# Kernel tuning notes

Measured on AMD Instinct MI355X. Metric: run time of the kernel, lower is better.

Reference implementation:

```python
import jax, jax.numpy as jnp
import numpy as np
import math

V, S, D, B = 50257, 2048, 512, 4
DFF = 4 * D
EPS = 1e-5


def layer_norm(z, g, b):
    mu = jnp.mean(z, axis=-1, keepdims=True)
    var = jnp.mean((z - mu) ** 2, axis=-1, keepdims=True)
    return (z - mu) * jax.lax.rsqrt(var + EPS) * g + b


def pos_embedding(seq_len, d_model):
    # Faithful to get_positional_value: angle = pos / 10000**(2*i/d), sin for even i, cos for odd i
    pos = jnp.arange(seq_len, dtype=jnp.float32)[:, None]          # [S,1]
    i = jnp.arange(d_model, dtype=jnp.float32)[None, :]            # [1,D]
    ang = pos / jnp.power(10000.0, 2.0 * i / d_model)              # [S,D]
    even = (jnp.arange(d_model) % 2 == 0)[None, :]
    return jnp.where(even, jnp.sin(ang), jnp.cos(ang))


def setup_inputs() -> dict:
    key = jax.random.key(0)
    ks = jax.random.split(key, 14)
    w = lambda k, sh: jax.random.normal(k, sh, dtype=jnp.float32) * 0.02
    return {
        "input_seq": jax.random.randint(ks[0], (B, S), 0, V),
        "emb": w(ks[1], (V, D)),
        "wk": w(ks[2], (D, D)), "bk": jnp.zeros((D,), jnp.float32),
        "wq": w(ks[3], (D, D)), "bq": jnp.zeros((D,), jnp.float32),
        "wv": w(ks[4], (D, D)), "bv": jnp.zeros((D,), jnp.float32),
        "ln_g": jnp.ones((D,), jnp.float32), "ln_b": jnp.zeros((D,), jnp.float32),
        "w1": w(ks[5], (D, DFF)), "b1": jnp.zeros((DFF,), jnp.float32),
        "w2": w(ks[6], (DFF, D)), "b2": jnp.zeros((D,), jnp.float32),
    }


def reference(input_seq, emb, wk, bk, wq, bq, wv, bv, ln_g, ln_b, w1, b1, w2, b2):
    x = emb[input_seq]                                              # [B,S,D]
    x = (x + pos_embedding(S, D)) * math.sqrt(D)
    # NB original passes (k, q, v) into Attention(Q, K, V), so Q:=k_proj, K:=q_proj, V:=v_proj
    k = x @ wk + bk
    q = x @ wq + bq
    v = x @ wv + bv
    scores = jnp.einsum("bid,bjd->bij", k, q) / math.sqrt(D)        # [B,S,S]
    attn = jax.nn.softmax(scores, axis=-1) @ v                      # [B,S,D]
    r = layer_norm(x + attn, ln_g, ln_b)
    ff = jax.nn.gelu(r @ w1 + b1, approximate=False) @ w2 + b2
    out = layer_norm(r + ff, ln_g, ln_b)                            # shared LN params (same module reused)
    return out
```

## Files before the change

### kernel.cpp

```cpp
#include <hip/hip_runtime.h>
#include <math.h>

static constexpr int BB  = 4;
static constexpr int S   = 2048;
static constexpr int D   = 512;
static constexpr int DFF = 2048;
static constexpr int BS  = BB * S;

using v8h = __attribute__((ext_vector_type(8))) _Float16;
using v4h = __attribute__((ext_vector_type(4))) _Float16;
using v2h = __attribute__((ext_vector_type(2))) _Float16;
using v4f = __attribute__((ext_vector_type(4))) float;

__device__ __forceinline__ void async16(const void* g, void* l) {
  __builtin_amdgcn_global_load_lds(
      (const __attribute__((address_space(1))) unsigned int*)g,
      (__attribute__((address_space(3))) unsigned int*)l, 16, 0, 0);
}

__device__ __forceinline__ float blockSum(float v) {
#pragma unroll
  for (int o = 32; o; o >>= 1) v += __shfl_xor(v, o, 64);
  __shared__ float t[4];
  __syncthreads();
  if ((threadIdx.x & 63) == 0) t[threadIdx.x >> 6] = v;
  __syncthreads();
  return t[0] + t[1] + t[2] + t[3];
}
__device__ __forceinline__ float blockMax(float v) {
#pragma unroll
  for (int o = 32; o; o >>= 1) v = fmaxf(v, __shfl_xor(v, o, 64));
  __shared__ float t[4];
  __syncthreads();
  if ((threadIdx.x & 63) == 0) t[threadIdx.x >> 6] = v;
  __syncthreads();
  return fmaxf(fmaxf(t[0], t[1]), fmaxf(t[2], t[3]));
}

__global__ __launch_bounds__(256) void embed_pos_k(
    const int* __restrict__ seq, const float* __restrict__ emb,
    float* __restrict__ X, _Float16* __restrict__ Xh) {
  const int bs = blockIdx.x;
  const int s  = bs & (S - 1);
  const int idx = seq[bs];
  const float* er = emb + (size_t)idx * D;
  const float cexp = -0.05190512648261504f;
  const int d0 = threadIdx.x * 2;
  const float2 e2 = *(const float2*)&er[d0];
  const float a0 = (float)s * exp2f((float)d0 * cexp);
  const float a1 = (float)s * exp2f((float)(d0 + 1) * cexp);
  const float v0 = (e2.x + sinf(a0)) * 22.62741699796952f;
  const float v1 = (e2.y + cosf(a1)) * 22.62741699796952f;
  const size_t o = (size_t)bs * D + d0;
  *(float2*)&X[o] = make_float2(v0, v1);
  *(v2h*)&Xh[o] = v2h{(_Float16)v0, (_Float16)v1};
}

__global__ __launch_bounds__(256) void prep_k(
    const float* __restrict__ wk, const float* __restrict__ wq,
    const float* __restrict__ wv, const float* __restrict__ w1,
    const float* __restrict__ w2, const float* __restrict__ bk,
    const float* __restrict__ bq, const float* __restrict__ bv,
    _Float16* __restrict__ wcat, _Float16* __restrict__ w1T,
    _Float16* __restrict__ w2T, float* __restrict__ bcat) {
  const int idx = blockIdx.x * 256 + threadIdx.x;
  if (idx < 786432) {
    const int which = idx >> 18, e = idx & 262143;
    const int k = e >> 9, n = e & 511;
    const float* w = (which == 0) ? wk : (which == 1) ? wq : wv;
    wcat[((long)(which * 512 + n)) * 512 + k] = (_Float16)w[e];
  } else if (idx < 786432 + 1048576) {
    const int e = idx - 786432;
    const int k = e >> 11, n = e & 2047;
    w1T[(long)n * 512 + k] = (_Float16)w1[e];
  } else if (idx < 786432 + 2097152) {
    const int e = idx - 786432 - 1048576;
    const int k = e >> 9, n = e & 511;
    w2T[(long)n * 2048 + k] = (_Float16)w2[e];
  } else if (idx < 786432 + 2097152 + 1536) {
    const int e = idx - 786432 - 2097152;
    const float* b = (e < 512) ? bk : (e < 1024) ? bq : bv;
    bcat[e] = b[e & 511];
  }
}

template <int OMODE, int ACT>
__global__ __launch_bounds__(512, 2) void mm256_k(
    const _Float16* __restrict__ Ap, const _Float16* __restrict__ Bp,
    void* __restrict__ Cp, void* __restrict__ Cp2, void* __restrict__ Cp3,
    const float* __restrict__ bias,
    int N, int K, long sA, long sB, long sC, float scale) {
  constexpr int ATE = 256 * 64;
  constexpr int TILE = 2 * ATE;
  __shared__ __align__(16) _Float16 lds[2 * TILE];

  const int tid = threadIdx.x, lane = tid & 63, w = tid >> 6;
  const int quad = lane >> 4, l16 = lane & 15;
  const int wm = w >> 2, wn = w & 3;
  const int m0 = blockIdx.y * 256, n0 = blockIdx.x * 256;

  const _Float16* A = Ap + (long)blockIdx.z * sA;
  const _Float16* B = Bp + (long)blockIdx.z * sB;

  v4f acc[8][4] = {};
  const int srow8 = lane >> 3;
  const int cs = (lane & 7) ^ srow8;
  const int lsw = l16 & 7;

  auto stage = [&](int k0, int half) {
    _Float16* Ah = lds + half * TILE;
    _Float16* Bh = Ah + ATE;
#pragma unroll
    for (int i = 0; i < 4; ++i) {
      const int is = w + i * 8;
      async16(A + (long)(m0 + is * 8 + srow8) * K + k0 + cs * 8, Ah + is * 512);
      async16(B + (long)(n0 + is * 8 + srow8) * K + k0 + cs * 8, Bh + is * 512);
    }
  };

  stage(0, 0);
  __syncthreads();

  const int nK = K >> 6;
  for (int t = 0; t < nK; ++t) {
    const int cur = t & 1;
    if (t + 1 < nK) stage((t + 1) << 6, cur ^ 1);

    const _Float16* Ah = lds + cur * TILE;
    const _Float16* Bh = Ah + ATE;

    v8h bfr[4][2];
#pragma unroll
    for (int nt = 0; nt < 4; ++nt) {
      const int rn = wn * 64 + nt * 16 + l16;
#pragma unroll
      for (int kk = 0; kk < 2; ++kk) {
        const int c = (kk * 4 + quad) ^ lsw;
        bfr[nt][kk] = *(v8h*)&Bh[rn * 64 + c * 8];
      }
    }
#pragma unroll
    for (int mt = 0; mt < 8; ++mt) {
      const int rr = wm * 128 + mt * 16 + l16;
      v8h af[2];
#pragma unroll
      for (int kk = 0; kk < 2; ++kk) {
        const int c = (kk * 4 + quad) ^ lsw;
        af[kk] = *(v8h*)&Ah[rr * 64 + c * 8];
      }
#pragma unroll
      for (int kk = 0; kk < 2; ++kk)
#pragma unroll
        for (int nt = 0; nt < 4; ++nt)
          acc[mt][nt] = __builtin_amdgcn_mfma_f32_16x16x32_f16(
              af[kk], bfr[nt][kk], acc[mt][nt], 0, 0, 0);
    }

    __syncthreads();
  }

  const long Cz = (long)blockIdx.z * sC;
  const int region = n0 >> 9;
#pragma unroll
  for (int nt = 0; nt < 4; ++nt) {
    const int gn = n0 + wn * 64 + nt * 16 + l16;
    const int gnl = gn & 511;
    const float bv = bias ? bias[gn] : 0.0f;
#pragma unroll
    for (int mt = 0; mt < 8; ++mt) {
      const int gmb = m0 + wm * 128 + mt * 16 + quad * 4;
      if constexpr (OMODE == 4) {
        if (region == 2) {
          const int z2 = gmb >> 11, ml = gmb & 2047;
          v4h h4;
#pragma unroll
          for (int r = 0; r < 4; ++r)
            h4[r] = (_Float16)(acc[mt][nt][r] * scale + bv);
          *(v4h*)&((_Float16*)Cp3)[((long)z2 * 512 + gnl) * 2048 + ml] = h4;
          continue;
        }
      }
#pragma unroll
      for (int r = 0; r < 4; ++r) {
        const int gm = gmb + r;
        float v = acc[mt][nt][r] * scale + bv;
        if constexpr (ACT == 1)
          v = 0.5f * v * (1.0f + erff(v * 0.7071067811865476f));
        if constexpr (OMODE == 1) {
          ((_Float16*)Cp)[Cz + (long)gm * N + gn] = (_Float16)v;
        } else {
          if (region == 0) {
            ((_Float16*)Cp)[(long)gm * 512 + gnl] = (_Float16)v;
          } else {
            ((_Float16*)Cp2)[(long)gm * 512 + gnl] = (_Float16)v;
          }
        }
      }
    }
  }
}

template <int TM, int OMODE, int ACT>
__global__ __launch_bounds__(256) void mm_k(
    const _Float16* __restrict__ Ap, const _Float16* __restrict__ Bp,
    void* __restrict__ Cp, void* __restrict__ Cp2, void* __restrict__ Cp3,
    const float* __restrict__ bias,
    int N, int K, long sA, long sB, long sC, float scale) {
  constexpr int ATE = TM * 64;
  constexpr int BTE = 128 * 64;
  constexpr int TILE = ATE + BTE;
  __shared__ __align__(16) _Float16 lds[2 * TILE];

  const int tid = threadIdx.x, lane = tid & 63, w = tid >> 6;
  const int quad = lane >> 4, l16 = lane & 15;
  constexpr int MT = 4;
  constexpr int NT = (TM == 128) ? 4 : 2;
  constexpr int WN = (TM == 128) ? 64 : 32;
  const int wm = (TM == 128) ? (w >> 1) : 0;
  const int wn = (TM == 128) ? (w & 1) : w;
  const int m0 = blockIdx.y * TM, n0 = blockIdx.x * 128;

  const _Float16* A = Ap + (long)blockIdx.z * sA;
  const _Float16* B = Bp + (long)blockIdx.z * sB;

  v4f acc[MT][NT] = {};
  const int srow8 = lane >> 3;
  const int cs = (lane & 7) ^ srow8;
  const int lsw = l16 & 7;

  auto stage = [&](int k0, int half) {
    _Float16* Ah = lds + half * TILE;
    _Float16* Bh = Ah + ATE;
#pragma unroll
    for (int i = 0; i < TM / 32; ++i) {
      const int is = w + i * 4;
      async16(A + (long)(m0 + is * 8 + srow8) * K + k0 + cs * 8, Ah + is * 512);
    }
#pragma unroll
    for (int i = 0; i < 4; ++i) {
      const int is = w + i * 4;
      async16(B + (long)(n0 + is * 8 + srow8) * K + k0 + cs * 8, Bh + is * 512);
    }
  };

  stage(0, 0);
  __syncthreads();

  const int nK = K >> 6;
  for (int t = 0; t < nK; ++t) {
    const int cur = t & 1;
    if (t + 1 < nK) stage((t + 1) << 6, cur ^ 1);

    const _Float16* Ah = lds + cur * TILE;
    const _Float16* Bh = Ah + ATE;

    v8h af[MT][2], bfr[NT][2];
#pragma unroll
    for (int mt = 0; mt < MT; ++mt) {
      const int rr = wm * 64 + mt * 16 + l16;
#pragma unroll
      for (int kk = 0; kk < 2; ++kk) {
        const int c = (kk * 4 + quad) ^ lsw;
        af[mt][kk] = *(v8h*)&Ah[rr * 64 + c * 8];
      }
    }
#pragma unroll
    for (int nt = 0; nt < NT; ++nt) {
      const int rn = wn * WN + nt * 16 + l16;
#pragma unroll
      for (int kk = 0; kk < 2; ++kk) {
        const int c = (kk * 4 + quad) ^ lsw;
        bfr[nt][kk] = *(v8h*)&Bh[rn * 64 + c * 8];
      }
    }
#pragma unroll
    for (int kk = 0; kk < 2; ++kk)
#pragma unroll
      for (int mt = 0; mt < MT; ++mt)
#pragma unroll
        for (int nt = 0; nt < NT; ++nt)
          acc[mt][nt] = __builtin_amdgcn_mfma_f32_16x16x32_f16(
              af[mt][kk], bfr[nt][kk], acc[mt][nt], 0, 0, 0);

    __syncthreads();
  }

  const long Cz = (long)blockIdx.z * sC;
#pragma unroll
  for (int nt = 0; nt < NT; ++nt) {
    const int gn = n0 + wn * WN + nt * 16 + l16;
    const float bv = bias ? bias[gn] : 0.0f;
#pragma unroll
    for (int mt = 0; mt < MT; ++mt) {
      const int gmb = m0 + wm * 64 + mt * 16 + quad * 4;
#pragma unroll
      for (int r = 0; r < 4; ++r) {
        const int gm = gmb + r;
        float v = acc[mt][nt][r] * scale + bv;
        if constexpr (ACT == 1)
          v = 0.5f * v * (1.0f + erff(v * 0.7071067811865476f));
        if constexpr (OMODE == 0) {
          ((float*)Cp)[Cz + (long)gm * N + gn] = v;
        } else {
          ((_Float16*)Cp)[Cz + (long)gm * N + gn] = (_Float16)v;
        }
      }
    }
  }
}

__global__ __launch_bounds__(256) void softmax_k(_Float16* __restrict__ Sc) {
  _Float16* p = Sc + (size_t)blockIdx.x * S;
  const int base = threadIdx.x * 8;
  const v8h a = *(const v8h*)(p + base);
  float v[8];
#pragma unroll
  for (int i = 0; i < 8; ++i) v[i] = (float)a[i];
  float m = -1e30f;
#pragma unroll
  for (int i = 0; i < 8; ++i) m = fmaxf(m, v[i]);
  m = blockMax(m);
  float sum = 0.f;
#pragma unroll
  for (int i = 0; i < 8; ++i) {
    v[i] = exp2f((v[i] - m) * 1.44269504f);
    sum += v[i];
  }
  sum = blockSum(sum);
  const float inv = 1.0f / sum;
  v8h o;
#pragma unroll
  for (int i = 0; i < 8; ++i) o[i] = (_Float16)(v[i] * inv);
  *(v8h*)(p + base) = o;
}

__global__ __launch_bounds__(256) void ln_res_k(
    float* __restrict__ X, const float* __restrict__ Add,
    const float* __restrict__ g, const float* __restrict__ b,
    _Float16* __restrict__ rF) {
  float* xr = X + (size_t)blockIdx.x * D;
  const float* ar = Add + (size_t)blockIdx.x * D;
  _Float16* rf = rF + (size_t)blockIdx.x * D;
  const int d0 = threadIdx.x * 2;
  const float2 xv = *(const float2*)&xr[d0];
  const float2 av = *(const float2*)&ar[d0];
  const float z0 = xv.x + av.x;
  const float z1 = xv.y + av.y;
  const float mu = blockSum(z0 + z1) * (1.0f / D);
  const float dd0 = z0 - mu, dd1 = z1 - mu;
  const float var = blockSum(dd0 * dd0 + dd1 * dd1) * (1.0f / D);
  const float rs = rsqrtf(var + 1e-5f);
  const float2 gv = *(const float2*)&g[d0];
  const float2 bv = *(const float2*)&b[d0];
  const float v0 = dd0 * rs * gv.x + bv.x;
  const float v1 = dd1 * rs * gv.y + bv.y;
  *(float2*)&xr[d0] = make_float2(v0, v1);
  *(v2h*)&rf[d0] = v2h{(_Float16)v0, (_Float16)v1};
}

__global__ __launch_bounds__(256) void ln_out_k(
    const float* __restrict__ R, const float* __restrict__ F,
    const float* __restrict__ g, const float* __restrict__ b,
    float* __restrict__ out) {
  const float* rr = R + (size_t)blockIdx.x * D;
  const float* fr = F + (size_t)blockIdx.x * D;
  float* orow = out + (size_t)blockIdx.x * D;
  const int d0 = threadIdx.x * 2;
  const float2 rv = *(const float2*)&rr[d0];
  const float2 fv = *(const float2*)&fr[d0];
  const float z0 = rv.x + fv.x;
  const float z1 = rv.y + fv.y;
  const float mu = blockSum(z0 + z1) * (1.0f / D);
  const float dd0 = z0 - mu, dd1 = z1 - mu;
  const float var = blockSum(dd0 * dd0 + dd1 * dd1) * (1.0f / D);
  const float rs = rsqrtf(var + 1e-5f);
  const float2 gv = *(const float2*)&g[d0];
  const float2 bv = *(const float2*)&b[d0];
  *(float2*)&orow[d0] =
      make_float2(dd0 * rs * gv.x + bv.x, dd1 * rs * gv.y + bv.y);
}

extern "C" void kernel_launch(void* const* d_in, const int* in_sizes, int n_in,
                              void* d_out, int out_size, void* d_ws, size_t ws_size,
                              hipStream_t stream) {
  (void)in_sizes; (void)n_in; (void)out_size; (void)ws_size;
  const int*   seq = (const int*)d_in[0];
  const float* emb = (const float*)d_in[1];
  const float* wk  = (const float*)d_in[2];
  const float* bk  = (const float*)d_in[3];
  const float* wq  = (const float*)d_in[4];
  const float* bq  = (const float*)d_in[5];
  const float* wv  = (const float*)d_in[6];
  const float* bv  = (const float*)d_in[7];
  const float* lng = (const float*)d_in[8];
  const float* lnb = (const float*)d_in[9];
  const float* w1  = (const float*)d_in[10];
  const float* b1  = (const float*)d_in[11];
  const float* w2  = (const float*)d_in[12];
  const float* b2  = (const float*)d_in[13];

  const size_t MBy = 1024 * 1024;
  char* wsb = (char*)d_ws;
  float*    X    = (float*)wsb;
  _Float16* Xh   = (_Float16*)(wsb + 16 * MBy);
  _Float16* kF   = (_Float16*)(wsb + 24 * MBy);
  _Float16* qF   = (_Float16*)(wsb + 32 * MBy);
  _Float16* vT   = (_Float16*)(wsb + 40 * MBy);
  _Float16* Sc   = (_Float16*)(wsb + 48 * MBy);
  float*    attn = (float*)(wsb + 81 * MBy);
  _Float16* rF   = (_Float16*)(wsb + 24 * MBy);
  _Float16* hF   = (_Float16*)(wsb + 48 * MBy);
  float*    ff   = (float*)(wsb + 32 * MBy);
  _Float16* wcat = (_Float16*)(wsb + 100 * MBy);
  float*    bcat = (float*)(wsb + 102 * MBy);
  _Float16* w1T  = (_Float16*)(wsb + 103 * MBy);
  _Float16* w2T  = (_Float16*)(wsb + 105 * MBy);

  const long SD = (long)S * D, SSl = (long)S * S;

  prep_k<<<11270, 256, 0, stream>>>(wk, wq, wv, w1, w2, bk, bq, bv,
                                    wcat, w1T, w2T, bcat);
  embed_pos_k<<<BS, 256, 0, stream>>>(seq, emb, X, Xh);

  mm256_k<4, 0><<<dim3(6, 32, 1), 512, 0, stream>>>(
      Xh, wcat, kF, qF, vT, bcat, 1536, D, 0, 0, 0, 1.0f);

  mm256_k<1, 0><<<dim3(8, 8, BB), 512, 0, stream>>>(
      kF, qF, Sc, nullptr, nullptr, nullptr, S, D, SD, SD, SSl,
      0.044194173824159216f);

  softmax_k<<<BS, 256, 0, stream>>>(Sc);

  mm_k<64, 0, 0><<<dim3(4, 32, BB), 256, 0, stream>>>(
      Sc, vT, attn, nullptr, nullptr, nullptr, D, S, SSl, (long)D * S, SD,
      1.0f);

  ln_res_k<<<BS, 256, 0, stream>>>(X, attn, lng, lnb, rF);

  mm256_k<1, 1><<<dim3(8, 32, 1), 512, 0, stream>>>(
      rF, w1T, hF, nullptr, nullptr, b1, DFF, D, 0, 0, 0, 1.0f);
  mm_k<64, 0, 0><<<dim3(4, 128, 1), 256, 0, stream>>>(
      hF, w2T, ff, nullptr, nullptr, b2, D, DFF, 0, 0, 0, 1.0f);

  ln_out_k<<<BS, 256, 0, stream>>>(X, ff, lng, lnb, (float*)d_out);
}
```

Before: 391.2 us.

## Replace 256-tile GEMMs with 128-tile kernel and add triple-buffered K-pipelined GEMM

Removes the 512-thread 256x256-tile GEMM and routes the QKV, QK^T and FFN1 products through the 128-row mm_k kernel, which gains the fused split-output epilogue. This launches more, smaller blocks. It also adds mm64p_k, a 64x128-tile GEMM with a three-stage LDS ring and explicit vmcnt waits, used for the long-K products (attn@V and FFN2) to overlap global loads with MFMA. The trade-off is less data reuse per block in exchange for better occupancy and latency hiding.

Result: faster. 365.6 us (-6.5%).

```diff
diff --git a/kernel.cpp b/kernel.cpp
--- a/kernel.cpp
+++ b/kernel.cpp
@@ -84,122 +84,6 @@
   }
 }
 
-template <int OMODE, int ACT>
-__global__ __launch_bounds__(512, 2) void mm256_k(
-    const _Float16* __restrict__ Ap, const _Float16* __restrict__ Bp,
-    void* __restrict__ Cp, void* __restrict__ Cp2, void* __restrict__ Cp3,
-    const float* __restrict__ bias,
-    int N, int K, long sA, long sB, long sC, float scale) {
-  constexpr int ATE = 256 * 64;
-  constexpr int TILE = 2 * ATE;
-  __shared__ __align__(16) _Float16 lds[2 * TILE];
-
-  const int tid = threadIdx.x, lane = tid & 63, w = tid >> 6;
-  const int quad = lane >> 4, l16 = lane & 15;
-  const int wm = w >> 2, wn = w & 3;
-  const int m0 = blockIdx.y * 256, n0 = blockIdx.x * 256;
-
-  const _Float16* A = Ap + (long)blockIdx.z * sA;
-  const _Float16* B = Bp + (long)blockIdx.z * sB;
-
-  v4f acc[8][4] = {};
-  const int srow8 = lane >> 3;
-  const int cs = (lane & 7) ^ srow8;
-  const int lsw = l16 & 7;
-
-  auto stage = [&](int k0, int half) {
-    _Float16* Ah = lds + half * TILE;
-    _Float16* Bh = Ah + ATE;
-#pragma unroll
-    for (int i = 0; i < 4; ++i) {
-      const int is = w + i * 8;
-      async16(A + (long)(m0 + is * 8 + srow8) * K + k0 + cs * 8, Ah + is * 512);
-      async16(B + (long)(n0 + is * 8 + srow8) * K + k0 + cs * 8, Bh + is * 512);
-    }
-  };
-
-  stage(0, 0);
-  __syncthreads();
-
-  const int nK = K >> 6;
-  for (int t = 0; t < nK; ++t) {
-    const int cur = t & 1;
-    if (t + 1 < nK) stage((t + 1) << 6, cur ^ 1);
-
-    const _Float16* Ah = lds + cur * TILE;
-    const _Float16* Bh = Ah + ATE;
-
-    v8h bfr[4][2];
-#pragma unroll
-    for (int nt = 0; nt < 4; ++nt) {
-      const int rn = wn * 64 + nt * 16 + l16;
-#pragma unroll
-      for (int kk = 0; kk < 2; ++kk) {
-        const int c = (kk * 4 + quad) ^ lsw;
-        bfr[nt][kk] = *(v8h*)&Bh[rn * 64 + c * 8];
-      }
-    }
-#pragma unroll
-    for (int mt = 0; mt < 8; ++mt) {
-      const int rr = wm * 128 + mt * 16 + l16;
-      v8h af[2];
-#pragma unroll
-      for (int kk = 0; kk < 2; ++kk) {
-        const int c = (kk * 4 + quad) ^ lsw;
-        af[kk] = *(v8h*)&Ah[rr * 64 + c * 8];
-      }
-#pragma unroll
-      for (int kk = 0; kk < 2; ++kk)
-#pragma unroll
-        for (int nt = 0; nt < 4; ++nt)
-          acc[mt][nt] = __builtin_amdgcn_mfma_f32_16x16x32_f16(
-              af[kk], bfr[nt][kk], acc[mt][nt], 0, 0, 0);
-    }
-
-    __syncthreads();
-  }
-
-  const long Cz = (long)blockIdx.z * sC;
-  const int region = n0 >> 9;
-#pragma unroll
-  for (int nt = 0; nt < 4; ++nt) {
-    const int gn = n0 + wn * 64 + nt * 16 + l16;
-    const int gnl = gn & 511;
-    const float bv = bias ? bias[gn] : 0.0f;
-#pragma unroll
-    for (int mt = 0; mt < 8; ++mt) {
-      const int gmb = m0 + wm * 128 + mt * 16 + quad * 4;
-      if constexpr (OMODE == 4) {
-        if (region == 2) {
-          const int z2 = gmb >> 11, ml = gmb & 2047;
-          v4h h4;
-#pragma unroll
-          for (int r = 0; r < 4; ++r)
-            h4[r] = (_Float16)(acc[mt][nt][r] * scale + bv);
-          *(v4h*)&((_Float16*)Cp3)[((long)z2 * 512 + gnl) * 2048 + ml] = h4;
-          continue;
-        }
-      }
-#pragma unroll
-      for (int r = 0; r < 4; ++r) {
-        const int gm = gmb + r;
-        float v = acc[mt][nt][r] * scale + bv;
-        if constexpr (ACT == 1)
-          v = 0.5f * v * (1.0f + erff(v * 0.7071067811865476f));
-        if constexpr (OMODE == 1) {
-          ((_Float16*)Cp)[Cz + (long)gm * N + gn] = (_Float16)v;
-        } else {
-          if (region == 0) {
-            ((_Float16*)Cp)[(long)gm * 512 + gnl] = (_Float16)v;
-          } else {
-            ((_Float16*)Cp2)[(long)gm * 512 + gnl] = (_Float16)v;
-          }
-        }
-      }
-    }
-  }
-}
-
 template <int TM, int OMODE, int ACT>
 __global__ __launch_bounds__(256) void mm_k(
     const _Float16* __restrict__ Ap, const _Float16* __restrict__ Bp,
@@ -286,13 +170,26 @@
   }
 
   const long Cz = (long)blockIdx.z * sC;
+  const int region = n0 >> 9;
 #pragma unroll
   for (int nt = 0; nt < NT; ++nt) {
     const int gn = n0 + wn * WN + nt * 16 + l16;
+    const int gnl = gn & 511;
     const float bv = bias ? bias[gn] : 0.0f;
 #pragma unroll
     for (int mt = 0; mt < MT; ++mt) {
       const int gmb = m0 + wm * 64 + mt * 16 + quad * 4;
+      if constexpr (OMODE == 4) {
+        if (region == 2) {
+          const int z2 = gmb >> 11, ml = gmb & 2047;
+          v4h h4;
+#pragma unroll
+          for (int r = 0; r < 4; ++r)
+            h4[r] = (_Float16)(acc[mt][nt][r] * scale + bv);
+          *(v4h*)&((_Float16*)Cp3)[((long)z2 * 512 + gnl) * 2048 + ml] = h4;
+          continue;
+        }
+      }
 #pragma unroll
       for (int r = 0; r < 4; ++r) {
         const int gm = gmb + r;
@@ -301,9 +198,117 @@
           v = 0.5f * v * (1.0f + erff(v * 0.7071067811865476f));
         if constexpr (OMODE == 0) {
           ((float*)Cp)[Cz + (long)gm * N + gn] = v;
+        } else if constexpr (OMODE == 1) {
+          ((_Float16*)Cp)[Cz + (long)gm * N + gn] = (_Float16)v;
         } else {
-          ((_Float16*)Cp)[Cz + (long)gm * N + gn] = (_Float16)v;
+          if (region == 0) {
+            ((_Float16*)Cp)[(long)gm * 512 + gnl] = (_Float16)v;
+          } else {
+            ((_Float16*)Cp2)[(long)gm * 512 + gnl] = (_Float16)v;
+          }
         }
+      }
+    }
+  }
+}
+
+__global__ __launch_bounds__(256) void mm64p_k(
+    const _Float16* __restrict__ Ap, const _Float16* __restrict__ Bp,
+    float* __restrict__ Cp, const float* __restrict__ bias,
+    int N, int K, long sA, long sB, long sC, float scale) {
+  constexpr int ATE = 64 * 64;
+  constexpr int BTE = 128 * 64;
+  constexpr int TILE = ATE + BTE;
+  __shared__ __align__(16) _Float16 lds[3 * TILE];
+
+  const int tid = threadIdx.x, lane = tid & 63, w = tid >> 6;
+  const int quad = lane >> 4, l16 = lane & 15;
+  const int m0 = blockIdx.y * 64, n0 = blockIdx.x * 128;
+
+  const _Float16* A = Ap + (long)blockIdx.z * sA;
+  const _Float16* B = Bp + (long)blockIdx.z * sB;
+
+  v4f acc[4][2] = {};
+  const int srow8 = lane >> 3;
+  const int cs = (lane & 7) ^ srow8;
+  const int lsw = l16 & 7;
+
+  auto stage = [&](int t) {
+    _Float16* Ah = lds + (t % 3) * TILE;
+    _Float16* Bh = Ah + ATE;
+    const int k0 = t << 6;
+#pragma unroll
+    for (int i = 0; i < 2; ++i) {
+      const int is = w + i * 4;
+      async16(A + (long)(m0 + is * 8 + srow8) * K + k0 + cs * 8, Ah + is * 512);
+    }
+#pragma unroll
+    for (int i = 0; i < 4; ++i) {
+      const int is = w + i * 4;
+      async16(B + (long)(n0 + is * 8 + srow8) * K + k0 + cs * 8, Bh + is * 512);
+    }
+  };
+
+  const int nK = K >> 6;
+  stage(0);
+  stage(1);
+
+  for (int t = 0; t < nK; ++t) {
+    __builtin_amdgcn_s_barrier();
+    if (t + 2 < nK) {
+      stage(t + 2);
+      asm volatile("s_waitcnt vmcnt(12)" ::: "memory");
+    } else if (t + 1 < nK) {
+      asm volatile("s_waitcnt vmcnt(6)" ::: "memory");
+    } else {
+      asm volatile("s_waitcnt vmcnt(0)" ::: "memory");
+    }
+    __builtin_amdgcn_s_barrier();
+
+    const _Float16* Ah = lds + (t % 3) * TILE;
+    const _Float16* Bh = Ah + ATE;
+
+    v8h af[4][2], bfr[2][2];
+#pragma unroll
+    for (int mt = 0; mt < 4; ++mt) {
+      const int rr = mt * 16 + l16;
+#pragma unroll
+      for (int kk = 0; kk < 2; ++kk) {
+        const int c = (kk * 4 + quad) ^ lsw;
+        af[mt][kk] = *(v8h*)&Ah[rr * 64 + c * 8];
+      }
+    }
+#pragma unroll
+    for (int nt = 0; nt < 2; ++nt) {
+      const int rn = w * 32 + nt * 16 + l16;
+#pragma unroll
+      for (int kk = 0; kk < 2; ++kk) {
+        const int c = (kk * 4 + quad) ^ lsw;
+        bfr[nt][kk] = *(v8h*)&Bh[rn * 64 + c * 8];
+      }
+    }
+#pragma unroll
+    for (int kk = 0; kk < 2; ++kk)
+#pragma unroll
+      for (int mt = 0; mt < 4; ++mt)
+#pragma unroll
+        for (int nt = 0; nt < 2; ++nt)
+          acc[mt][nt] = __builtin_amdgcn_mfma_f32_16x16x32_f16(
+              af[mt][kk], bfr[nt][kk], acc[mt][nt], 0, 0, 0);
+  }
+
+  const long Cz = (long)blockIdx.z * sC;
+#pragma unroll
+  for (int nt = 0; nt < 2; ++nt) {
+    const int gn = n0 + w * 32 + nt * 16 + l16;
+    const float bv = bias ? bias[gn] : 0.0f;
+#pragma unroll
+    for (int mt = 0; mt < 4; ++mt) {
+      const int gmb = m0 + mt * 16 + quad * 4;
+#pragma unroll
+      for (int r = 0; r < 4; ++r) {
+        const int gm = gmb + r;
+        Cp[Cz + (long)gm * N + gn] = acc[mt][nt][r] * scale + bv;
       }
     }
   }
@@ -422,25 +427,24 @@
                                     wcat, w1T, w2T, bcat);
   embed_pos_k<<<BS, 256, 0, stream>>>(seq, emb, X, Xh);
 
-  mm256_k<4, 0><<<dim3(6, 32, 1), 512, 0, stream>>>(
+  mm_k<128, 4, 0><<<dim3(12, 64, 1), 256, 0, stream>>>(
       Xh, wcat, kF, qF, vT, bcat, 1536, D, 0, 0, 0, 1.0f);
 
-  mm256_k<1, 0><<<dim3(8, 8, BB), 512, 0, stream>>>(
+  mm_k<128, 1, 0><<<dim3(16, 16, BB), 256, 0, stream>>>(
       kF, qF, Sc, nullptr, nullptr, nullptr, S, D, SD, SD, SSl,
       0.044194173824159216f);
 
   softmax_k<<<BS, 256, 0, stream>>>(Sc);
 
-  mm_k<64, 0, 0><<<dim3(4, 32, BB), 256, 0, stream>>>(
-      Sc, vT, attn, nullptr, nullptr, nullptr, D, S, SSl, (long)D * S, SD,
-      1.0f);
+  mm64p_k<<<dim3(4, 32, BB), 256, 0, stream>>>(
+      Sc, vT, attn, nullptr, D, S, SSl, (long)D * S, SD, 1.0f);
 
   ln_res_k<<<BS, 256, 0, stream>>>(X, attn, lng, lnb, rF);
 
-  mm256_k<1, 1><<<dim3(8, 32, 1), 512, 0, stream>>>(
+  mm_k<128, 1, 1><<<dim3(16, 64, 1), 256, 0, stream>>>(
       rF, w1T, hF, nullptr, nullptr, b1, DFF, D, 0, 0, 0, 1.0f);
-  mm_k<64, 0, 0><<<dim3(4, 128, 1), 256, 0, stream>>>(
-      hF, w2T, ff, nullptr, nullptr, b2, D, DFF, 0, 0, 0, 1.0f);
+  mm64p_k<<<dim3(4, 128, 1), 256, 0, stream>>>(
+      hF, w2T, ff, b2, D, DFF, 0, 0, 0, 1.0f);
 
   ln_out_k<<<BS, 256, 0, stream>>>(X, ff, lng, lnb, (float*)d_out);
 }
```
